# Kernel optimization log

Hardware: AMD Instinct MI355X
Metric: run time of the kernel (lower is better)

The kernel has to match this reference:

```python
import jax, jax.numpy as jnp
import numpy as np


def setup_inputs() -> dict:
    key = jax.random.key(0)
    k1, k2, k3 = jax.random.split(key, 3)
    L, B, H = 256, 8, 512
    inputs = jax.random.normal(k1, (L, B, H), dtype=jnp.float32)
    attn_W = jax.random.normal(k2, (H, 2 * H), dtype=jnp.float32) * 0.02
    attn_b = jnp.zeros((H,), dtype=jnp.float32)
    score_W = jax.random.normal(k3, (1, H), dtype=jnp.float32) * 0.02
    score_b = jnp.zeros((1,), dtype=jnp.float32)
    return {"inputs": inputs, "attn_W": attn_W, "attn_b": attn_b,
            "score_W": score_W, "score_b": score_b}


def reference(inputs, attn_W, attn_b, score_W, score_b):
    # inputs: [L, B, H]; attn_W: [H, 2H] (torch Linear weight), attn_b: [H]
    # score_W: [1, H], score_b: [1]
    H = attn_W.shape[0]
    # Decompose Linear(cat(sen1, sen2)) = sen1 @ W1^T + sen2 @ W2^T + b
    W1 = attn_W[:, :H]   # [H, H] acts on sen1 (row index i)
    W2 = attn_W[:, H:]   # [H, H] acts on sen2 (col index j)
    x = jnp.transpose(inputs, (1, 0, 2))          # [B, L, H]
    p1 = jnp.einsum('blh,oh->blo', x, W1)         # [B, L, H]
    p2 = jnp.einsum('blh,oh->blo', x, W2)         # [B, L, H]
    # feat[b,i,j,:] = tanh(attn(cat(x[b,i], x[b,j])))  -> [B, L, L, H]
    feat = jnp.tanh(p1[:, :, None, :] + p2[:, None, :, :] + attn_b)
    # score Linear H -> 1, squeeze last dim -> [B, L, L]
    energies = jnp.einsum('bijh,h->bij', feat, score_W[0]) + score_b[0]
    # softmax over dim=1 (the sen1 / i axis), as in the torch code
    return jax.nn.softmax(energies, axis=1)
```

## Files before the change

### kernel.cpp

```cpp
#include <hip/hip_runtime.h>

#define LOG2E 1.4426950408889634f
#define SCALE (2.0f * LOG2E)

__device__ __forceinline__ float fast_exp2(float x) { return __builtin_amdgcn_exp2f(x); }
__device__ __forceinline__ float fast_rcp(float x)  { return __builtin_amdgcn_rcpf(x); }

typedef __attribute__((ext_vector_type(8))) short bf16x8;
typedef __attribute__((ext_vector_type(4))) float f32x4;

__device__ __forceinline__ void cvt_hilo8(const float* vv, ushort* hi8, ushort* lo8) {
#pragma unroll
    for (int j = 0; j < 8; ++j) {
        unsigned u32 = __float_as_uint(vv[j]);
        unsigned h = (u32 + 0x7FFF + ((u32 >> 16) & 1)) >> 16;
        hi8[j] = (ushort)h;
        float lo = vv[j] - __uint_as_float(h << 16);
        unsigned ul = __float_as_uint(lo);
        lo8[j] = (ushort)((ul + 0x7FFF + ((ul >> 16) & 1)) >> 16);
    }
}

__global__ __launch_bounds__(512) void mfma_gemm(const float* __restrict__ inputs,
                                                 const float* __restrict__ attn_W,
                                                 const float* __restrict__ attn_b,
                                                 float* __restrict__ E1,
                                                 float* __restrict__ E2) {
    const int xcd = blockIdx.x & 7;
    const int idx = blockIdx.x >> 3;
    const int mb  = xcd * 2 + (idx >> 4);
    const int nb  = idx & 15;
    __shared__ ushort lds[24576];
    ushort* const Ahi = lds;
    ushort* const Alo = lds + 8192;
    ushort* const Bhi = lds + 16384;
    ushort* const Blo = lds + 20480;

    const int t = threadIdx.x;
    const int lane = t & 63, w = t >> 6;
    const int wr = w >> 1, wc = w & 1;

    const int arow0 = t >> 3, ak8 = t & 7;
    const int arow1 = (t + 512) >> 3;
    const int m0 = mb * 128 + arow0;
    const int m1 = mb * 128 + arow1;
    const float* asrc0 = inputs + (long)((m0 & 255) * 8 + (m0 >> 8)) * 512 + ak8 * 8;
    const float* asrc1 = inputs + (long)((m1 & 255) * 8 + (m1 >> 8)) * 512 + ak8 * 8;
    const int nloc = t >> 3, bk8 = t & 7;
    const int ngl = nb * 64 + nloc;
    const float* bsrc = attn_W + (long)(ngl & 511) * 1024 + (ngl >> 9) * 512 + bk8 * 8;

    const int aoff0 = (arow0 >> 6) * 4096 + (ak8 >> 2) * 2048 + ((arow0 & 63) >> 4) * 512 +
                      ((ak8 & 3) * 16 + (arow0 & 15)) * 8;
    const int aoff1 = (arow1 >> 6) * 4096 + (ak8 >> 2) * 2048 + ((arow1 & 63) >> 4) * 512 +
                      ((ak8 & 3) * 16 + (arow1 & 15)) * 8;
    const int boff  = (bk8 >> 2) * 2048 + (nloc >> 4) * 512 +
                      ((bk8 & 3) * 16 + (nloc & 15)) * 8;

    f32x4 acc[2][2];
#pragma unroll
    for (int i = 0; i < 2; ++i)
#pragma unroll
        for (int j = 0; j < 2; ++j)
            acc[i][j] = (f32x4){0.f, 0.f, 0.f, 0.f};

    float ra0[8], ra1[8], rb[8];
#define LOADF(ss)                                                              \
    {                                                                          \
        *(float4*)&ra0[0] = *(const float4*)(asrc0 + (ss) * 64);               \
        *(float4*)&ra0[4] = *(const float4*)(asrc0 + (ss) * 64 + 4);           \
        *(float4*)&ra1[0] = *(const float4*)(asrc1 + (ss) * 64);               \
        *(float4*)&ra1[4] = *(const float4*)(asrc1 + (ss) * 64 + 4);           \
        *(float4*)&rb[0]  = *(const float4*)(bsrc  + (ss) * 64);               \
        *(float4*)&rb[4]  = *(const float4*)(bsrc  + (ss) * 64 + 4);           \
    }

    LOADF(0);

    for (int ss = 0; ss < 8; ++ss) {
        __syncthreads();
        {
            ushort h8[8], l8[8];
            cvt_hilo8(ra0, h8, l8);
            *(uint4*)&Ahi[aoff0] = *(const uint4*)h8;
            *(uint4*)&Alo[aoff0] = *(const uint4*)l8;
            cvt_hilo8(ra1, h8, l8);
            *(uint4*)&Ahi[aoff1] = *(const uint4*)h8;
            *(uint4*)&Alo[aoff1] = *(const uint4*)l8;
            cvt_hilo8(rb, h8, l8);
            *(uint4*)&Bhi[boff] = *(const uint4*)h8;
            *(uint4*)&Blo[boff] = *(const uint4*)l8;
        }
        if (ss < 7) LOADF(ss + 1);
        __syncthreads();

#pragma unroll
        for (int pass = 0; pass < 3; ++pass) {
            const ushort* Ab = (pass == 1) ? Alo : Ahi;
            const ushort* Bb = (pass == 2) ? Blo : Bhi;
#pragma unroll
            for (int ks = 0; ks < 2; ++ks) {
                bf16x8 a[2], b[2];
                const int abase = (wr >> 1) * 4096 + ks * 2048 + (wr & 1) * 1024 + lane * 8;
                const int bbase = ks * 2048 + wc * 1024 + lane * 8;
                a[0] = *(const bf16x8*)&Ab[abase];
                a[1] = *(const bf16x8*)&Ab[abase + 512];
                b[0] = *(const bf16x8*)&Bb[bbase];
                b[1] = *(const bf16x8*)&Bb[bbase + 512];
#pragma unroll
                for (int mf = 0; mf < 2; ++mf)
#pragma unroll
                    for (int nf = 0; nf < 2; ++nf)
                        acc[mf][nf] = __builtin_amdgcn_mfma_f32_16x16x32_bf16(
                            a[mf], b[nf], acc[mf][nf], 0, 0, 0);
            }
        }
    }
#undef LOADF

#pragma unroll
    for (int nf = 0; nf < 2; ++nf) {
        int n = nb * 64 + wc * 32 + nf * 16 + (lane & 15);
        const bool isE1 = (n < 512);
        float* dst = isE1 ? E1 : E2;
        int o = n & 511;
        float bias = isE1 ? attn_b[o] : 0.0f;
#pragma unroll
        for (int mf = 0; mf < 2; ++mf) {
            int ml = mb * 128 + wr * 32 + mf * 16 + ((lane >> 4) << 2);
            int bb = ml >> 8, l = ml & 255;
            long rowoff = ((long)(bb * 8 + (l >> 5)) * 512 + o) * 32 + (l & 31);
#pragma unroll
            for (int r = 0; r < 4; ++r)
                dst[rowoff + r] = fast_exp2(SCALE * (acc[mf][nf][r] + bias));
        }
    }
}

__global__ __launch_bounds__(256) void energy_kernel(const float* __restrict__ E1,
                                                     const float* __restrict__ E2,
                                                     const float* __restrict__ sW,
                                                     float* __restrict__ EP) {
    const int bid = blockIdx.x;
    const int tj = bid & 3;
    const int ti = (bid >> 2) & 3;
    const int b  = (bid >> 4) & 7;
    const int s  = bid >> 7;
    __shared__ float As[32 * 64];
    __shared__ float Bs[32 * 64];
    __shared__ float csh[128];

    const int t = threadIdx.x;
    const int tx = t & 15, ty = t >> 4;

    if (t < 128) csh[t] = 2.0f * sW[s * 128 + t];

    const float* e1base = E1 + (long)(b * 8 + ti * 2) * 16384;
    const float* e2base = E2 + (long)(b * 8 + tj * 2) * 16384;

    float acc[4][4];
#pragma unroll
    for (int i = 0; i < 4; ++i)
#pragma unroll
        for (int j = 0; j < 4; ++j) acc[i][j] = 0.f;

    for (int c0 = 0; c0 < 128; c0 += 32) {
        __syncthreads();
#pragma unroll
        for (int it = 0; it < 2; ++it) {
            const int f = it * 256 + t;
            const int ol = f >> 4;
            const int i4 = (f & 15) * 4;
            const long srcoff = (long)(i4 >> 5) * 16384 + (long)(s * 128 + c0 + ol) * 32 + (i4 & 31);
            *(float4*)&As[ol * 64 + i4] = *(const float4*)(e1base + srcoff);
            *(float4*)&Bs[ol * 64 + i4] = *(const float4*)(e2base + srcoff);
        }
        __syncthreads();

#pragma unroll 2
        for (int p = 0; p < 8; ++p) {
            const float4 c4 = *(const float4*)&csh[c0 + p * 4];
            float4 a0 = *(const float4*)&As[(p * 4 + 0) * 64 + ty * 4];
            float4 a1 = *(const float4*)&As[(p * 4 + 1) * 64 + ty * 4];
            float4 a2 = *(const float4*)&As[(p * 4 + 2) * 64 + ty * 4];
            float4 a3 = *(const float4*)&As[(p * 4 + 3) * 64 + ty * 4];
            float4 b0 = *(const float4*)&Bs[(p * 4 + 0) * 64 + tx * 4];
            float4 b1 = *(const float4*)&Bs[(p * 4 + 1) * 64 + tx * 4];
            float4 b2 = *(const float4*)&Bs[(p * 4 + 2) * 64 + tx * 4];
            float4 b3 = *(const float4*)&Bs[(p * 4 + 3) * 64 + tx * 4];
            const float a0v[4] = {a0.x, a0.y, a0.z, a0.w};
            const float a1v[4] = {a1.x, a1.y, a1.z, a1.w};
            const float a2v[4] = {a2.x, a2.y, a2.z, a2.w};
            const float a3v[4] = {a3.x, a3.y, a3.z, a3.w};
            const float b0v[4] = {b0.x, b0.y, b0.z, b0.w};
            const float b1v[4] = {b1.x, b1.y, b1.z, b1.w};
            const float b2v[4] = {b2.x, b2.y, b2.z, b2.w};
            const float b3v[4] = {b3.x, b3.y, b3.z, b3.w};
#pragma unroll
            for (int i = 0; i < 4; ++i) {
#pragma unroll
                for (int j = 0; j < 4; ++j) {
                    float y0 = fmaf(a0v[i], b0v[j], 1.0f);
                    float y1 = fmaf(a1v[i], b1v[j], 1.0f);
                    float y2 = fmaf(a2v[i], b2v[j], 1.0f);
                    float y3 = fmaf(a3v[i], b3v[j], 1.0f);
                    float y01 = y0 * y1, y23 = y2 * y3;
                    float d = y01 * y23;
                    float n01 = fmaf(c4.x, y1, c4.y * y0);
                    float n23 = fmaf(c4.z, y3, c4.w * y2);
                    float n = fmaf(n01, y23, n23 * y01);
                    acc[i][j] = fmaf(n, fast_rcp(d), acc[i][j]);
                }
            }
        }
    }

    float* Eb = EP + (long)s * 524288 + (long)b * 65536 +
                (long)(ti * 64 + ty * 4) * 256 + tj * 64 + tx * 4;
#pragma unroll
    for (int i = 0; i < 4; ++i)
        *(float4*)&Eb[i * 256] = make_float4(acc[i][0], acc[i][1], acc[i][2], acc[i][3]);
}

__global__ __launch_bounds__(256) void softmax_kernel(const float* __restrict__ P0,
                                                      const float* __restrict__ P1,
                                                      const float* __restrict__ P2,
                                                      const float* __restrict__ P3,
                                                      float* __restrict__ out) {
    const int b  = blockIdx.x >> 4;
    const int jt = blockIdx.x & 15;
    const int t  = threadIdx.x;
    const int jx = t & 15;
    const int iy = t >> 4;
    const long base = (long)b * 65536 + jt * 16 + jx;

    float v[16];
#pragma unroll
    for (int k = 0; k < 16; ++k) {
        long idx = base + (long)(iy + k * 16) * 256;
        v[k] = -(P0[idx] + P1[idx] + P2[idx] + P3[idx]);
    }

    float m = v[0];
#pragma unroll
    for (int k = 1; k < 16; ++k) m = fmaxf(m, v[k]);

    __shared__ float red[256];
    red[t] = m;
    __syncthreads();
    if (t < 128) red[t] = fmaxf(red[t], red[t + 128]);
    __syncthreads();
    if (t < 64) red[t] = fmaxf(red[t], red[t + 64]);
    __syncthreads();
    if (t < 32) red[t] = fmaxf(red[t], red[t + 32]);
    __syncthreads();
    if (t < 16) red[t] = fmaxf(red[t], red[t + 16]);
    __syncthreads();
    m = red[jx];
    __syncthreads();

    float ssum = 0.f;
#pragma unroll
    for (int k = 0; k < 16; ++k) {
        v[k] = fast_exp2((v[k] - m) * LOG2E);
        ssum += v[k];
    }
    red[t] = ssum;
    __syncthreads();
    if (t < 128) red[t] += red[t + 128];
    __syncthreads();
    if (t < 64) red[t] += red[t + 64];
    __syncthreads();
    if (t < 32) red[t] += red[t + 32];
    __syncthreads();
    if (t < 16) red[t] += red[t + 16];
    __syncthreads();
    float inv = fast_rcp(red[jx]);

#pragma unroll
    for (int k = 0; k < 16; ++k) {
        long idx = base + (long)(iy + k * 16) * 256;
        out[idx] = v[k] * inv;
    }
}

extern "C" void kernel_launch(void* const* d_in, const int* in_sizes, int n_in,
                              void* d_out, int out_size, void* d_ws, size_t ws_size,
                              hipStream_t stream) {
    const float* inputs  = (const float*)d_in[0];
    const float* attn_W  = (const float*)d_in[1];
    const float* attn_b  = (const float*)d_in[2];
    const float* score_W = (const float*)d_in[3];
    float* out = (float*)d_out;

    float* ws = (float*)d_ws;
    float* E1 = ws;
    float* E2 = ws + (1 << 20);
    float* EP = ws + (2 << 20);

    mfma_gemm<<<256, 512, 0, stream>>>(inputs, attn_W, attn_b, E1, E2);
    energy_kernel<<<512, 256, 0, stream>>>(E1, E2, score_W, EP);
    softmax_kernel<<<128, 256, 0, stream>>>(EP, EP + 524288, EP + 2 * 524288,
                                            EP + 3 * 524288, out);
}
```

Before: 53.42 us.

## Fuse softmax into energy kernel via last-block atomic counter

Removes the separate softmax launch. Each energy block increments a per-(batch, column-tile) counter after writing its partial energies, and the 16th block to arrive sums the four partials and does the column softmax over all 256 rows for its 64 columns. This saves a kernel launch and the inter-kernel gap, but it adds a memset launch. Only 32 blocks do the softmax, each thread with 64 serial strided loads and a 64-float register array, so that tail may be slow and may raise register pressure for the whole kernel.

```diff
diff --git a/kernel.cpp b/kernel.cpp
--- a/kernel.cpp
+++ b/kernel.cpp
@@ -140,7 +140,9 @@
 __global__ __launch_bounds__(256) void energy_kernel(const float* __restrict__ E1,
                                                      const float* __restrict__ E2,
                                                      const float* __restrict__ sW,
-                                                     float* __restrict__ EP) {
+                                                     float* __restrict__ EP,
+                                                     unsigned* __restrict__ cnt,
+                                                     float* __restrict__ out) {
     const int bid = blockIdx.x;
     const int tj = bid & 3;
     const int ti = (bid >> 2) & 3;
@@ -149,6 +151,7 @@
     __shared__ float As[32 * 64];
     __shared__ float Bs[32 * 64];
     __shared__ float csh[128];
+    __shared__ unsigned lastflag;
 
     const int t = threadIdx.x;
     const int tx = t & 15, ty = t >> 4;
@@ -220,67 +223,50 @@
 #pragma unroll
     for (int i = 0; i < 4; ++i)
         *(float4*)&Eb[i * 256] = make_float4(acc[i][0], acc[i][1], acc[i][2], acc[i][3]);
-}
-
-__global__ __launch_bounds__(256) void softmax_kernel(const float* __restrict__ P0,
-                                                      const float* __restrict__ P1,
-                                                      const float* __restrict__ P2,
-                                                      const float* __restrict__ P3,
-                                                      float* __restrict__ out) {
-    const int b  = blockIdx.x >> 4;
-    const int jt = blockIdx.x & 15;
-    const int t  = threadIdx.x;
-    const int jx = t & 15;
-    const int iy = t >> 4;
-    const long base = (long)b * 65536 + jt * 16 + jx;
-
-    float v[16];
-#pragma unroll
-    for (int k = 0; k < 16; ++k) {
-        long idx = base + (long)(iy + k * 16) * 256;
-        v[k] = -(P0[idx] + P1[idx] + P2[idx] + P3[idx]);
-    }
-
-    float m = v[0];
-#pragma unroll
-    for (int k = 1; k < 16; ++k) m = fmaxf(m, v[k]);
-
-    __shared__ float red[256];
-    red[t] = m;
+
+    __threadfence();
+    if (t == 0) lastflag = atomicAdd(&cnt[b * 4 + tj], 1u);
     __syncthreads();
-    if (t < 128) red[t] = fmaxf(red[t], red[t + 128]);
-    __syncthreads();
-    if (t < 64) red[t] = fmaxf(red[t], red[t + 64]);
-    __syncthreads();
-    if (t < 32) red[t] = fmaxf(red[t], red[t + 32]);
-    __syncthreads();
-    if (t < 16) red[t] = fmaxf(red[t], red[t + 16]);
-    __syncthreads();
-    m = red[jx];
-    __syncthreads();
-
-    float ssum = 0.f;
-#pragma unroll
-    for (int k = 0; k < 16; ++k) {
-        v[k] = fast_exp2((v[k] - m) * LOG2E);
-        ssum += v[k];
-    }
-    red[t] = ssum;
-    __syncthreads();
-    if (t < 128) red[t] += red[t + 128];
-    __syncthreads();
-    if (t < 64) red[t] += red[t + 64];
-    __syncthreads();
-    if (t < 32) red[t] += red[t + 32];
-    __syncthreads();
-    if (t < 16) red[t] += red[t + 16];
-    __syncthreads();
-    float inv = fast_rcp(red[jx]);
-
-#pragma unroll
-    for (int k = 0; k < 16; ++k) {
-        long idx = base + (long)(iy + k * 16) * 256;
-        out[idx] = v[k] * inv;
+    if (lastflag == 15) {
+        __threadfence();
+        const int jl = t & 63;
+        const int q  = t >> 6;
+        const int jcol = tj * 64 + jl;
+        const float* base0 = EP + (long)b * 65536 + jcol;
+        float v[64];
+        float m = -3.0e38f;
+#pragma unroll
+        for (int k = 0; k < 64; ++k) {
+            const long idx = (long)(q * 64 + k) * 256;
+            float sum = base0[idx] + base0[524288 + idx] +
+                        base0[1048576 + idx] + base0[1572864 + idx];
+            v[k] = -sum;
+            m = fmaxf(m, v[k]);
+        }
+        float* red = As;
+        red[t] = m;
+        __syncthreads();
+        if (t < 64)
+            red[t] = fmaxf(fmaxf(red[t], red[t + 64]), fmaxf(red[t + 128], red[t + 192]));
+        __syncthreads();
+        m = red[jl];
+        float ssum = 0.f;
+#pragma unroll
+        for (int k = 0; k < 64; ++k) {
+            v[k] = fast_exp2((v[k] - m) * LOG2E);
+            ssum += v[k];
+        }
+        __syncthreads();
+        red[t] = ssum;
+        __syncthreads();
+        if (t < 64)
+            red[t] = (red[t] + red[t + 64]) + (red[t + 128] + red[t + 192]);
+        __syncthreads();
+        const float inv = fast_rcp(red[jl]);
+        float* ob = out + (long)b * 65536 + jcol;
+#pragma unroll
+        for (int k = 0; k < 64; ++k)
+            ob[(long)(q * 64 + k) * 256] = v[k] * inv;
     }
 }
 
@@ -297,9 +283,9 @@
     float* E1 = ws;
     float* E2 = ws + (1 << 20);
     float* EP = ws + (2 << 20);
-
+    unsigned* cnt = (unsigned*)(ws + (4 << 20));
+
+    hipMemsetAsync((void*)cnt, 0, 32 * sizeof(unsigned), stream);
     mfma_gemm<<<256, 512, 0, stream>>>(inputs, attn_W, attn_b, E1, E2);
-    energy_kernel<<<512, 256, 0, stream>>>(E1, E2, score_W, EP);
-    softmax_kernel<<<128, 256, 0, stream>>>(EP, EP + 524288, EP + 2 * 524288,
-                                            EP + 3 * 524288, out);
-}
+    energy_kernel<<<512, 256, 0, stream>>>(E1, E2, score_W, EP, cnt, out);
+}
```

Measured after the change: 145.9 us. 173% more time.
